# Performance work log

Hardware: AMD Instinct MI355X
Metric: run time of the kernel (lower is better)

Reference implementation:

```python
import jax, jax.numpy as jnp
from jax import lax
import numpy as np

D, DI, S, K, R = 128, 256, 16, 4, 8  # d_model, d_inner, d_state, d_conv, dt_rank
B, W, N, E = 8, 64, 128, 256


def _ln(x, g, b, eps=1e-5):
    m = x.mean(-1, keepdims=True)
    v = ((x - m) ** 2).mean(-1, keepdims=True)
    return (x - m) * lax.rsqrt(v + eps) * g + b


def _mamba(x, w_in, conv_w, conv_b, w_xp, dt_w, dt_b, Alog, Dp, w_out):
    # x: (Bq, W, D) -> (Bq, W, D). Faithful mamba_ssm.Mamba math (selective scan).
    Bq, Wlen, _ = x.shape
    xz = x @ w_in                       # (Bq, W, 2*DI)
    xc, z = jnp.split(xz, 2, axis=-1)
    # causal depthwise conv over time
    xt = xc.transpose(0, 2, 1)          # (Bq, DI, W)
    xt = lax.conv_general_dilated(xt, conv_w[:, None, :], (1,), [(K - 1, 0)],
                                  feature_group_count=DI)
    xc = jax.nn.silu(xt + conv_b[None, :, None]).transpose(0, 2, 1)  # (Bq, W, DI)
    dbc = xc @ w_xp                     # (Bq, W, R+2S)
    dt = jax.nn.softplus(dbc[..., :R] @ dt_w + dt_b)   # (Bq, W, DI)
    Bm = dbc[..., R:R + S]              # (Bq, W, S)
    Cm = dbc[..., R + S:]               # (Bq, W, S)
    A = -jnp.exp(Alog)                  # (DI, S)

    def step(h, inp):
        dt_t, B_t, C_t, x_t = inp       # (Bq,DI),(Bq,S),(Bq,S),(Bq,DI)
        dA = jnp.exp(dt_t[..., None] * A)                 # (Bq,DI,S)
        h = dA * h + (dt_t * x_t)[..., None] * B_t[:, None, :]
        y = jnp.einsum('bds,bs->bd', h, C_t)
        return h, y

    h0 = jnp.zeros((Bq, DI, S), x.dtype)
    _, ys = lax.scan(step, h0, (dt.transpose(1, 0, 2), Bm.transpose(1, 0, 2),
                                Cm.transpose(1, 0, 2), xc.transpose(1, 0, 2)))
    y = ys.transpose(1, 0, 2) + xc * Dp          # D skip connection
    y = y * jax.nn.silu(z)
    return y @ w_out


def _forward(x_node, x_trace, x_log, mp_in, mp_conv_w, mp_conv_b, mp_xproj,
             mp_dt_w, mp_dt_b, mp_Alog, mp_D, mp_out, mix_w, mix_b,
             an_g, an_b, ff1_w, ff1_b, ff2_w, ff2_b, fln_g, fln_b):
    Bz, Wz, Nz, _ = x_node.shape
    Ez = x_trace.shape[2]
    # (B,W,N,D) -> (B*N, W, D) per-entity temporal sequences
    sn = x_node.transpose(0, 2, 1, 3).reshape(Bz * Nz, Wz, D)
    st = x_trace.transpose(0, 2, 1, 3).reshape(Bz * Ez, Wz, D)
    sl = x_log.transpose(0, 2, 1, 3).reshape(Bz * Nz, Wz, D)

    def mam(i, s):
        return _mamba(s, mp_in[i], mp_conv_w[i], mp_conv_b[i], mp_xproj[i],
                      mp_dt_w[i], mp_dt_b[i], mp_Alog[i], mp_D[i], mp_out[i])

    yn, yt, yl = mam(0, sn), mam(1, st), mam(2, sl)

    # cross-modal mixing of node & log with residual (dropout = identity in eval)
    cat = jnp.concatenate([yn, yl], axis=-1)          # (B*N, W, 2D)
    cat = cat + jax.nn.silu(cat @ mix_w + mix_b)
    yn, yl = jnp.split(cat, 2, axis=-1)

    # back to (B, W, N/E, D)
    yn = yn.reshape(Bz, Nz, Wz, D).transpose(0, 2, 1, 3)
    yt = yt.reshape(Bz, Ez, Wz, D).transpose(0, 2, 1, 3)
    yl = yl.reshape(Bz, Nz, Wz, D).transpose(0, 2, 1, 3)

    # AddALL: AddNorm(old, new) = LN(dropout(new) + old)
    n1 = _ln(yn + x_node, an_g[0], an_b[0])
    t1 = _ln(yt + x_trace, an_g[1], an_b[1])
    l1 = _ln(yl + x_log, an_g[2], an_b[2])

    # FFN: AddNorm(x, FeedForward(x)) per modality, LeakyReLU(0.01)
    def ffn(i, x):
        h = jax.nn.leaky_relu(x @ ff1_w[i] + ff1_b[i], 0.01)
        return _ln(h @ ff2_w[i] + ff2_b[i] + x, fln_g[i], fln_b[i])

    n2, t2, l2 = ffn(0, n1), ffn(1, t1), ffn(2, l1)
    # concat along entity axis (all feature dims = D) for a single output
    return jnp.concatenate([n2, t2, l2], axis=2)      # (B, W, 2N+E, D)


def setup_inputs() -> dict:
    key = jax.random.key(0)
    ks = jax.random.split(key, 16)
    f = lambda k, shp, s=1.0: jax.random.normal(k, shp, dtype=jnp.float32) * s
    return {
        'x_node': f(ks[0], (B, W, N, D)),
        'x_trace': f(ks[1], (B, W, E, D)),
        'x_log': f(ks[2], (B, W, N, D)),
        'mp_in': f(ks[3], (3, D, 2 * DI), 0.05),
        'mp_conv_w': f(ks[4], (3, DI, K), 0.2),
        'mp_conv_b': jnp.zeros((3, DI), jnp.float32),
        'mp_xproj': f(ks[5], (3, DI, R + 2 * S), 0.05),
        'mp_dt_w': f(ks[6], (3, R, DI), 0.1),
        'mp_dt_b': jnp.full((3, DI), float(np.log(np.expm1(0.01))), jnp.float32),
        'mp_Alog': jnp.log(jnp.broadcast_to(jnp.arange(1, S + 1, dtype=jnp.float32), (3, DI, S))),
        'mp_D': jnp.ones((3, DI), jnp.float32),
        'mp_out': f(ks[7], (3, DI, D), 0.05),
        'mix_w': f(ks[8], (2 * D, 2 * D), 0.05),
        'mix_b': jnp.zeros((2 * D,), jnp.float32),
        'an_g': jnp.ones((3, D), jnp.float32),
        'an_b': jnp.zeros((3, D), jnp.float32),
        'ff1_w': f(ks[9], (3, D, 4 * D), 0.05),
        'ff1_b': jnp.zeros((3, 4 * D), jnp.float32),
        'ff2_w': f(ks[10], (3, 4 * D, D), 0.05),
        'ff2_b': jnp.zeros((3, D), jnp.float32),
        'fln_g': jnp.ones((3, D), jnp.float32),
        'fln_b': jnp.zeros((3, D), jnp.float32),
    }


def reference(x_node, x_trace, x_log, mp_in, mp_conv_w, mp_conv_b, mp_xproj,
              mp_dt_w, mp_dt_b, mp_Alog, mp_D, mp_out, mix_w, mix_b,
              an_g, an_b, ff1_w, ff1_b, ff2_w, ff2_b, fln_g, fln_b):
    return _forward(x_node, x_trace, x_log, mp_in, mp_conv_w, mp_conv_b,
                    mp_xproj, mp_dt_w, mp_dt_b, mp_Alog, mp_D, mp_out,
                    mix_w, mix_b, an_g, an_b, ff1_w, ff1_b, ff2_w, ff2_b,
                    fln_g, fln_b)
```

## Files before the change

kernel.cpp:

```cpp
#include <hip/hip_runtime.h>
#include <hip/hip_bf16.h>

#define DEV __device__ __forceinline__

typedef __attribute__((ext_vector_type(8))) short bf16x8;
typedef __attribute__((ext_vector_type(4))) float f32x4;
typedef __attribute__((ext_vector_type(2))) float f32x2;

DEV f32x4 MF(bf16x8 a, bf16x8 b, f32x4 c) {
  return __builtin_amdgcn_mfma_f32_16x16x32_bf16(a, b, c, 0, 0, 0);
}

DEV float bf2f(unsigned short u) {
  union { unsigned int i; float f; } v; v.i = ((unsigned int)u) << 16; return v.f;
}
DEV unsigned short f2bf(float f) {
  __hip_bfloat16 h = __float2bfloat16(f);
  unsigned short r; __builtin_memcpy(&r, &h, 2); return r;
}
DEV unsigned int packbf(float a, float b) {
  float2 p; p.x = a; p.y = b;
  __hip_bfloat162 h = __float22bfloat162_rn(p);
  unsigned int r; __builtin_memcpy(&r, &h, 4); return r;
}
#define LOG2E 1.442695041f
#define LN2   0.6931471806f
DEV float silu_fast(float v) {
  float e = __builtin_amdgcn_exp2f(v * -LOG2E);
  return v * __builtin_amdgcn_rcpf(1.f + e);
}
DEV float softplus_fast(float v) {
  float e = __builtin_amdgcn_exp2f(v * LOG2E);
  float l = __builtin_amdgcn_logf(1.f + e) * LN2;
  return v > 15.f ? v : l;
}

#define WS_WINT   0
#define WS_WXPT   196608
#define WS_WOUTT  233472
#define WS_FF1T   331776
#define WS_FF2T   528384
#define WS_MIXT   724992
#define WS_TOTAL  790528

__global__ __launch_bounds__(256) void prep_kernel(
    const float* __restrict__ w_in, const float* __restrict__ w_xp,
    const float* __restrict__ w_out, const float* __restrict__ ff1,
    const float* __restrict__ ff2, const float* __restrict__ mixw,
    unsigned short* __restrict__ ws)
{
  int idx = blockIdx.x * 256 + threadIdx.x;
  if (idx >= WS_TOTAL) return;
  float v;
  if (idx < WS_WXPT) {
    int j = idx, s = j / 65536, r = j % 65536, n = r >> 7, k = r & 127;
    v = w_in[s * 65536 + k * 512 + n];
  } else if (idx < WS_WOUTT) {
    int j = idx - WS_WXPT, s = j / 12288, r = j % 12288, n = r >> 8, k = r & 255;
    v = (n < 40) ? w_xp[s * 10240 + k * 40 + n] : 0.f;
  } else if (idx < WS_FF1T) {
    int j = idx - WS_WOUTT, s = j / 32768, r = j % 32768, n = r >> 8, k = r & 255;
    v = w_out[s * 32768 + k * 128 + n];
  } else if (idx < WS_FF2T) {
    int j = idx - WS_FF1T, s = j / 65536, r = j % 65536, n = r >> 7, k = r & 127;
    v = ff1[s * 65536 + k * 512 + n];
  } else if (idx < WS_MIXT) {
    int j = idx - WS_FF2T, s = j / 65536, r = j % 65536, n = r >> 9, k = r & 511;
    v = ff2[s * 65536 + k * 128 + n];
  } else {
    int j = idx - WS_MIXT, n = j >> 8, k = j & 255;
    v = mixw[k * 256 + n];
  }
  ws[idx] = f2bf(v);
}

__global__ __launch_bounds__(256, 2) void mamba_front(
    const float* __restrict__ xn, const float* __restrict__ xt,
    const float* __restrict__ xl,
    const unsigned short* __restrict__ w_inT_all,
    const float* __restrict__ conv_w_all, const float* __restrict__ conv_b_all,
    const unsigned short* __restrict__ w_xpT_all,
    const float* __restrict__ dt_w_all, const float* __restrict__ dt_b_all,
    const float* __restrict__ Alog_all, const float* __restrict__ Dp_all,
    const unsigned short* __restrict__ w_outT_all,
    const float* __restrict__ an_g, const float* __restrict__ an_b,
    float* __restrict__ out)
{
  __shared__ __attribute__((aligned(16))) unsigned short xcz[64 * 512];
  __shared__ __attribute__((aligned(16))) char aux[16384];
  unsigned short* xs = (unsigned short*)aux;
  float* dbc = (float*)aux;

  const int tid = threadIdx.x;
  const int lane = tid & 63;
  const int wv = tid >> 6;
  const int lr = lane & 15;
  const int kg = lane >> 4;

  int blk = blockIdx.x, s, q;
  if (blk < 1024)      { s = 0; q = blk; }
  else if (blk < 3072) { s = 1; q = blk - 1024; }
  else                 { s = 2; q = blk - 3072; }
  const int SEQ = (s == 1) ? 256 : 128;
  const int slot_base = (s == 0) ? 0 : (s == 1 ? 128 : 384);
  const float* x = (s == 0) ? xn : (s == 1 ? xt : xl);
  const unsigned short* w_inT  = w_inT_all  + (size_t)s * 65536;
  const unsigned short* w_xpT  = w_xpT_all  + (size_t)s * 12288;
  const unsigned short* w_outT = w_outT_all + (size_t)s * 32768;
  const float* conv_w = conv_w_all + s * 1024;
  const float* conv_b = conv_b_all + s * 256;
  const float* dt_w   = dt_w_all + s * 2048;
  const float* dt_b   = dt_b_all + s * 256;
  const float* Alog   = Alog_all + s * 4096;
  const float* Dp     = Dp_all + s * 256;

  const int b = q / SEQ, n = q - b * SEQ;
  const float* xb = x + ((size_t)b * 64 * SEQ + n) * 128;

  for (int idx = tid; idx < 2048; idx += 256) {
    int t = idx >> 5, qd = (idx & 31) << 2;
    float4 v = *(const float4*)(xb + (size_t)t * SEQ * 128 + qd);
    uint2 p;
    p.x = packbf(v.x, v.y);
    p.y = packbf(v.z, v.w);
    *(uint2*)(&xs[t * 128 + (qd ^ ((t & 7) << 3))]) = p;
  }
  __syncthreads();

  {
    bf16x8 bx[4][4];
#pragma unroll
    for (int jt = 0; jt < 4; ++jt)
#pragma unroll
      for (int ks = 0; ks < 4; ++ks) {
        int t = jt * 16 + lr;
        bx[jt][ks] = *(const bf16x8*)(&xs[t * 128 + ((ks * 32 + kg * 8) ^ ((t & 7) << 3))]);
      }
    const int nb = wv * 128;
#pragma unroll
    for (int at = 0; at < 8; ++at) {
      bf16x8 av[4];
      int arow = nb + at * 16 + lr;
#pragma unroll
      for (int ks = 0; ks < 4; ++ks)
        av[ks] = *(const bf16x8*)(w_inT + arow * 128 + ks * 32 + kg * 8);
#pragma unroll
      for (int jt = 0; jt < 4; ++jt) {
        f32x4 c = {0.f, 0.f, 0.f, 0.f};
#pragma unroll
        for (int ks = 0; ks < 4; ++ks) c = MF(av[ks], bx[jt][ks], c);
        int t = jt * 16 + lr;
        int n0 = nb + at * 16 + kg * 4;
        uint2 p;
        p.x = packbf(c[0], c[1]);
        p.y = packbf(c[2], c[3]);
        *(uint2*)(&xcz[t * 512 + (n0 ^ ((t & 7) << 3))]) = p;
      }
    }
  }
  __syncthreads();

  {
    const int d = tid;
    float cw0 = conv_w[d * 4 + 0], cw1 = conv_w[d * 4 + 1];
    float cw2 = conv_w[d * 4 + 2], cw3 = conv_w[d * 4 + 3];
    float cb = conv_b[d];
    float xm3 = 0.f, xm2 = 0.f, xm1 = 0.f;
    for (int c0 = 0; c0 < 64; c0 += 16) {
      float xv[16];
#pragma unroll
      for (int u = 0; u < 16; ++u) {
        int t = c0 + u;
        xv[u] = bf2f(xcz[t * 512 + (d ^ ((t & 7) << 3))]);
      }
#pragma unroll
      for (int u = 0; u < 16; ++u) {
        float sv = fmaf(cw0, xm3, fmaf(cw1, xm2, fmaf(cw2, xm1, fmaf(cw3, xv[u], cb))));
        xm3 = xm2; xm2 = xm1; xm1 = xv[u];
        xv[u] = silu_fast(sv);
      }
#pragma unroll
      for (int u = 0; u < 16; ++u) {
        int t = c0 + u;
        xcz[t * 512 + (d ^ ((t & 7) << 3))] = f2bf(xv[u]);
      }
    }
  }
  __syncthreads();

  {
    bf16x8 av[8];
    int ta = wv * 16 + lr;
#pragma unroll
    for (int ks = 0; ks < 8; ++ks)
      av[ks] = *(const bf16x8*)(&xcz[ta * 512 + ((ks * 32 + kg * 8) ^ ((ta & 7) << 3))]);
#pragma unroll
    for (int ct = 0; ct < 3; ++ct) {
      f32x4 c = {0.f, 0.f, 0.f, 0.f};
#pragma unroll
      for (int ks = 0; ks < 8; ++ks) {
        bf16x8 bv = *(const bf16x8*)(w_xpT + (ct * 16 + lr) * 256 + ks * 32 + kg * 8);
        c = MF(av[ks], bv, c);
      }
      int tt = wv * 16 + kg * 4;
#pragma unroll
      for (int r = 0; r < 4; ++r)
        dbc[(tt + r) * 48 + ct * 16 + lr] = c[r];
    }
  }
  __syncthreads();

  {
    const int d = tid;
    float dtw[8];
#pragma unroll
    for (int r = 0; r < 8; ++r) dtw[r] = dt_w[r * 256 + d];
    const float dtb = dt_b[d];
    float Af2[16];
#pragma unroll
    for (int s2 = 0; s2 < 16; ++s2)
      Af2[s2] = -__builtin_amdgcn_exp2f(Alog[d * 16 + s2] * LOG2E) * LOG2E;
    const float af0l2 = Af2[0];
    bool geo = true;
#pragma unroll
    for (int s2 = 1; s2 < 16; ++s2)
      geo = geo && (fabsf(Af2[s2] - (float)(s2 + 1) * af0l2) <= 2e-4f * fabsf(Af2[s2]));
    const float Dv = Dp[d];

    const int eoff = d;
    const int zoff = 256 + d;

    if (geo) {
      f32x2 h2[8];
#pragma unroll
      for (int k = 0; k < 8; ++k) h2[k] = (f32x2){0.f, 0.f};
#pragma unroll 2
      for (int t = 0; t < 64; ++t) {
        const f32x4* dr4 = (const f32x4*)&dbc[t * 48];
        f32x4 d0 = dr4[0], d1 = dr4[1];
        float dtv = dtb;
        dtv = fmaf(dtw[0], d0[0], dtv); dtv = fmaf(dtw[1], d0[1], dtv);
        dtv = fmaf(dtw[2], d0[2], dtv); dtv = fmaf(dtw[3], d0[3], dtv);
        dtv = fmaf(dtw[4], d1[0], dtv); dtv = fmaf(dtw[5], d1[1], dtv);
        dtv = fmaf(dtw[6], d1[2], dtv); dtv = fmaf(dtw[7], d1[3], dtv);
        dtv = softplus_fast(dtv);
        int sw = (t & 7) << 3;
        int e = t * 512 + (eoff ^ sw);
        float xv = bf2f(xcz[e]);
        float zf = bf2f(xcz[t * 512 + (zoff ^ sw)]);
        float cf = dtv * xv;
        float r1 = __builtin_amdgcn_exp2f(dtv * af0l2);
        float r2 = r1 * r1;
        f32x2 r2v = {r2, r2};
        f32x2 pp = {r1, r2};
        f32x2 cf2 = {cf, cf};
        f32x2 y2 = {0.f, 0.f};
        f32x4 B0 = dr4[2], B1 = dr4[3], B2 = dr4[4], B3 = dr4[5];
        f32x4 C0 = dr4[6], C1 = dr4[7], C2 = dr4[8], C3 = dr4[9];
        f32x2 Bv[8] = {{B0[0],B0[1]},{B0[2],B0[3]},{B1[0],B1[1]},{B1[2],B1[3]},
                       {B2[0],B2[1]},{B2[2],B2[3]},{B3[0],B3[1]},{B3[2],B3[3]}};
        f32x2 Cv[8] = {{C0[0],C0[1]},{C0[2],C0[3]},{C1[0],C1[1]},{C1[2],C1[3]},
                       {C2[0],C2[1]},{C2[2],C2[3]},{C3[0],C3[1]},{C3[2],C3[3]}};
#pragma unroll
        for (int k = 0; k < 8; ++k) {
          h2[k] = __builtin_elementwise_fma(pp, h2[k], cf2 * Bv[k]);
          y2 = __builtin_elementwise_fma(h2[k], Cv[k], y2);
          pp = pp * r2v;
        }
        float y = y2[0] + y2[1];
        xcz[e] = f2bf((fmaf(xv, Dv, y)) * silu_fast(zf));
      }
    } else {
      float h[16];
#pragma unroll
      for (int s2 = 0; s2 < 16; ++s2) h[s2] = 0.f;
#pragma unroll 2
      for (int t = 0; t < 64; ++t) {
        const float* dr = &dbc[t * 48];
        float dtv = dtb;
#pragma unroll
        for (int r = 0; r < 8; ++r) dtv = fmaf(dtw[r], dr[r], dtv);
        dtv = softplus_fast(dtv);
        int sw = (t & 7) << 3;
        int e = t * 512 + (eoff ^ sw);
        float xv = bf2f(xcz[e]);
        float zf = bf2f(xcz[t * 512 + (zoff ^ sw)]);
        float cf = dtv * xv;
        float y = 0.f;
#pragma unroll
        for (int s2 = 0; s2 < 16; ++s2) {
          float dA = __builtin_amdgcn_exp2f(dtv * Af2[s2]);
          h[s2] = fmaf(dA, h[s2], cf * dr[8 + s2]);
          y = fmaf(h[s2], dr[24 + s2], y);
        }
        xcz[e] = f2bf((fmaf(xv, Dv, y)) * silu_fast(zf));
      }
    }
  }
  __syncthreads();

  {
    bf16x8 av[8];
    int ta = wv * 16 + lr;
#pragma unroll
    for (int ks = 0; ks < 8; ++ks)
      av[ks] = *(const bf16x8*)(&xcz[ta * 512 + ((ks * 32 + kg * 8) ^ ((ta & 7) << 3))]);
    f32x4 acc[8];
#pragma unroll
    for (int ct = 0; ct < 8; ++ct) {
      f32x4 c = {0.f, 0.f, 0.f, 0.f};
#pragma unroll
      for (int ks = 0; ks < 8; ++ks) {
        bf16x8 bv = *(const bf16x8*)(w_outT + (ct * 16 + lr) * 256 + ks * 32 + kg * 8);
        c = MF(av[ks], bv, c);
      }
      acc[ct] = c;
    }
    size_t ob = (size_t)b * 64 * 512 * 128 + (size_t)(slot_base + n) * 128;
    const int trow = wv * 16 + kg * 4;
    if (s != 1) {
#pragma unroll
      for (int ct = 0; ct < 8; ++ct) {
        int cc = ct * 16 + lr;
#pragma unroll
        for (int r = 0; r < 4; ++r)
          out[ob + (size_t)(trow + r) * 65536 + cc] = acc[ct][r];
      }
    } else {
      float sum[4] = {0.f, 0.f, 0.f, 0.f}, sq[4] = {0.f, 0.f, 0.f, 0.f};
#pragma unroll
      for (int ct = 0; ct < 8; ++ct) {
        int col = ct * 16 + lr;
#pragma unroll
        for (int r = 0; r < 4; ++r) {
          int t = trow + r;
          float xr = xb[(size_t)t * SEQ * 128 + col];
          float v = acc[ct][r] + xr;
          acc[ct][r] = v;
          sum[r] += v; sq[r] += v * v;
        }
      }
      float mn[4], rstd[4];
#pragma unroll
      for (int r = 0; r < 4; ++r) {
        float s1 = sum[r], s2 = sq[r];
        s1 += __shfl_xor(s1, 1); s2 += __shfl_xor(s2, 1);
        s1 += __shfl_xor(s1, 2); s2 += __shfl_xor(s2, 2);
        s1 += __shfl_xor(s1, 4); s2 += __shfl_xor(s2, 4);
        s1 += __shfl_xor(s1, 8); s2 += __shfl_xor(s2, 8);
        float mean = s1 * (1.f / 128.f);
        float var = s2 * (1.f / 128.f) - mean * mean;
        mn[r] = mean;
        rstd[r] = rsqrtf(var + 1e-5f);
      }
      const float* G  = an_g + 128;
      const float* Bv = an_b + 128;
#pragma unroll
      for (int ct = 0; ct < 8; ++ct) {
        int col = ct * 16 + lr;
        float gc = G[col], bc = Bv[col];
#pragma unroll
        for (int r = 0; r < 4; ++r)
          out[ob + (size_t)(trow + r) * 65536 + col] = (acc[ct][r] - mn[r]) * rstd[r] * gc + bc;
      }
    }
  }
}

__global__ __launch_bounds__(256, 4) void mix_kernel(
    float* __restrict__ out, const unsigned short* __restrict__ mixT,
    const float* __restrict__ mix_b,
    const float* __restrict__ xn, const float* __restrict__ xl,
    const float* __restrict__ an_g, const float* __restrict__ an_b)
{
  __shared__ __attribute__((aligned(16))) unsigned short cs[64 * 256];

  const int tid = threadIdx.x;
  const int lane = tid & 63;
  const int wv = tid >> 6;
  const int lr = lane & 15;
  const int kg = lane >> 4;
  const int bn = blockIdx.x;
  const int b = bn >> 7, n = bn & 127;
  const size_t base_n = (((size_t)b * 64) * 512 + n) * 128;
  const size_t base_l = (((size_t)b * 64) * 512 + 384 + n) * 128;

  for (int idx = tid; idx < 4096; idx += 256) {
    int t = idx >> 6, r = idx & 63;
    int half = r >> 5, qd = (r & 31) << 2;
    const float* src = out + (half ? base_l : base_n) + (size_t)t * 65536 + qd;
    float4 v = *(const float4*)src;
    int col = half * 128 + qd;
    uint2 p;
    p.x = packbf(v.x, v.y);
    p.y = packbf(v.z, v.w);
    *(uint2*)(&cs[t * 256 + (col ^ ((t & 7) << 3))]) = p;
  }
  __syncthreads();

  bf16x8 av[8];
  int ta = wv * 16 + lr;
#pragma unroll
  for (int ks = 0; ks < 8; ++ks)
    av[ks] = *(const bf16x8*)(&cs[ta * 256 + ((ks * 32 + kg * 8) ^ ((ta & 7) << 3))]);

  const int trow = wv * 16 + kg * 4;
#pragma unroll
  for (int half = 0; half < 2; ++half) {
    const float* xres_base = half ? xl : xn;
    f32x4 acc[8];
#pragma unroll
    for (int ct = 0; ct < 8; ++ct) {
      f32x4 c = {0.f, 0.f, 0.f, 0.f};
      int colg = half * 128 + ct * 16 + lr;
#pragma unroll
      for (int ks = 0; ks < 8; ++ks) {
        bf16x8 bv = *(const bf16x8*)(mixT + colg * 256 + ks * 32 + kg * 8);
        c = MF(av[ks], bv, c);
      }
      acc[ct] = c;
    }
    float sum[4] = {0.f, 0.f, 0.f, 0.f}, sq[4] = {0.f, 0.f, 0.f, 0.f};
#pragma unroll
    for (int ct = 0; ct < 8; ++ct) {
      int col = ct * 16 + lr;
      int colg = half * 128 + col;
      float bcol = mix_b[colg];
#pragma unroll
      for (int r = 0; r < 4; ++r) {
        int t = trow + r;
        float orig = bf2f(cs[t * 256 + (colg ^ ((t & 7) << 3))]);
        float xr = xres_base[(((size_t)b * 64 + t) * 128 + n) * 128 + col];
        float v = orig + silu_fast(acc[ct][r] + bcol) + xr;
        acc[ct][r] = v;
        sum[r] += v; sq[r] += v * v;
      }
    }
    float mn[4], rstd[4];
#pragma unroll
    for (int r = 0; r < 4; ++r) {
      float s1 = sum[r], s2 = sq[r];
      s1 += __shfl_xor(s1, 1); s2 += __shfl_xor(s2, 1);
      s1 += __shfl_xor(s1, 2); s2 += __shfl_xor(s2, 2);
      s1 += __shfl_xor(s1, 4); s2 += __shfl_xor(s2, 4);
      s1 += __shfl_xor(s1, 8); s2 += __shfl_xor(s2, 8);
      float mean = s1 * (1.f / 128.f);
      float var = s2 * (1.f / 128.f) - mean * mean;
      mn[r] = mean;
      rstd[r] = rsqrtf(var + 1e-5f);
    }
    const float* G  = an_g + (half ? 256 : 0);
    const float* Bv = an_b + (half ? 256 : 0);
    size_t base = half ? base_l : base_n;
#pragma unroll
    for (int ct = 0; ct < 8; ++ct) {
      int col = ct * 16 + lr;
      float gc = G[col], bc = Bv[col];
#pragma unroll
      for (int r = 0; r < 4; ++r)
        out[base + (size_t)(trow + r) * 65536 + col] = (acc[ct][r] - mn[r]) * rstd[r] * gc + bc;
    }
  }
}

__global__ __launch_bounds__(256, 2) void ffn_kernel(
    float* __restrict__ out,
    const unsigned short* __restrict__ ff1T, const float* __restrict__ b1,
    const unsigned short* __restrict__ ff2T, const float* __restrict__ b2,
    const float* __restrict__ g, const float* __restrict__ bb)
{
  __shared__ __attribute__((aligned(16))) unsigned short hT[64 * 512];
  __shared__ __attribute__((aligned(16))) unsigned short xs[64 * 128];

  const int tid = threadIdx.x;
  const int lane = tid & 63;
  const int wv = tid >> 6;
  const int lr = lane & 15;
  const int kg = lane >> 4;
  const int tok0 = blockIdx.x * 64;
  const int slot0 = tok0 & 511;
  const int s = slot0 < 128 ? 0 : (slot0 < 384 ? 1 : 2);
  const unsigned short* F1 = ff1T + (size_t)s * 65536;
  const unsigned short* F2 = ff2T + (size_t)s * 65536;
  const float* B1 = b1 + s * 512;
  const float* B2 = b2 + s * 128;
  const float* G = g + s * 128;
  const float* Bb = bb + s * 128;

  for (int idx = tid; idx < 2048; idx += 256) {
    int t = idx >> 5, qd = (idx & 31) << 2;
    float4 v = *(const float4*)(out + (size_t)(tok0 + t) * 128 + qd);
    uint2 p;
    p.x = packbf(v.x, v.y);
    p.y = packbf(v.z, v.w);
    *(uint2*)(&xs[t * 128 + (qd ^ ((t & 7) << 3))]) = p;
  }
  __syncthreads();

  {
    bf16x8 bx[4][4];
#pragma unroll
    for (int jt = 0; jt < 4; ++jt)
#pragma unroll
      for (int ks = 0; ks < 4; ++ks) {
        int t = jt * 16 + lr;
        bx[jt][ks] = *(const bf16x8*)(&xs[t * 128 + ((ks * 32 + kg * 8) ^ ((t & 7) << 3))]);
      }
    const int nb = wv * 128;
#pragma unroll
    for (int at = 0; at < 8; ++at) {
      bf16x8 av[4];
      int arow = nb + at * 16 + lr;
#pragma unroll
      for (int ks = 0; ks < 4; ++ks)
        av[ks] = *(const bf16x8*)(F1 + arow * 128 + ks * 32 + kg * 8);
      float4 bias = *(const float4*)(B1 + nb + at * 16 + kg * 4);
#pragma unroll
      for (int jt = 0; jt < 4; ++jt) {
        f32x4 c = {0.f, 0.f, 0.f, 0.f};
#pragma unroll
        for (int ks = 0; ks < 4; ++ks) c = MF(av[ks], bx[jt][ks], c);
        float v0 = c[0] + bias.x; v0 = v0 > 0.f ? v0 : 0.01f * v0;
        float v1 = c[1] + bias.y; v1 = v1 > 0.f ? v1 : 0.01f * v1;
        float v2 = c[2] + bias.z; v2 = v2 > 0.f ? v2 : 0.01f * v2;
        float v3 = c[3] + bias.w; v3 = v3 > 0.f ? v3 : 0.01f * v3;
        int t = jt * 16 + lr;
        int n0 = nb + at * 16 + kg * 4;
        uint2 p;
        p.x = packbf(v0, v1);
        p.y = packbf(v2, v3);
        *(uint2*)(&hT[t * 512 + (n0 ^ ((t & 7) << 3))]) = p;
      }
    }
  }
  __syncthreads();

  {
    bf16x8 av[16];
    int ta = wv * 16 + lr;
#pragma unroll
    for (int ks = 0; ks < 16; ++ks)
      av[ks] = *(const bf16x8*)(&hT[ta * 512 + ((ks * 32 + kg * 8) ^ ((ta & 7) << 3))]);
    f32x4 acc[8];
#pragma unroll
    for (int ct = 0; ct < 8; ++ct) {
      f32x4 c = {0.f, 0.f, 0.f, 0.f};
#pragma unroll
      for (int ks = 0; ks < 16; ++ks) {
        bf16x8 bv = *(const bf16x8*)(F2 + (ct * 16 + lr) * 512 + ks * 32 + kg * 8);
        c = MF(av[ks], bv, c);
      }
      acc[ct] = c;
    }

    float v[8][4];
    float sum[4] = {0.f, 0.f, 0.f, 0.f}, sq[4] = {0.f, 0.f, 0.f, 0.f};
    const int trow = wv * 16 + kg * 4;
#pragma unroll
    for (int ct = 0; ct < 8; ++ct) {
      int col = ct * 16 + lr;
      float b2c = B2[col];
#pragma unroll
      for (int r = 0; r < 4; ++r) {
        int t = trow + r;
        float xr = bf2f(xs[t * 128 + (col ^ ((t & 7) << 3))]);
        float val = acc[ct][r] + b2c + xr;
        v[ct][r] = val;
        sum[r] += val; sq[r] += val * val;
      }
    }
    float mn[4], rstd[4];
#pragma unroll
    for (int r = 0; r < 4; ++r) {
      float s1 = sum[r], s2 = sq[r];
      s1 += __shfl_xor(s1, 1); s2 += __shfl_xor(s2, 1);
      s1 += __shfl_xor(s1, 2); s2 += __shfl_xor(s2, 2);
      s1 += __shfl_xor(s1, 4); s2 += __shfl_xor(s2, 4);
      s1 += __shfl_xor(s1, 8); s2 += __shfl_xor(s2, 8);
      float mean = s1 * (1.f / 128.f);
      float var = s2 * (1.f / 128.f) - mean * mean;
      mn[r] = mean;
      rstd[r] = rsqrtf(var + 1e-5f);
    }
#pragma unroll
    for (int ct = 0; ct < 8; ++ct) {
      int col = ct * 16 + lr;
      float gc = G[col], bc = Bb[col];
#pragma unroll
      for (int r = 0; r < 4; ++r)
        out[(size_t)(tok0 + trow + r) * 128 + col] = (v[ct][r] - mn[r]) * rstd[r] * gc + bc;
    }
  }
}

extern "C" void kernel_launch(void* const* d_in, const int* in_sizes, int n_in,
                              void* d_out, int out_size, void* d_ws, size_t ws_size,
                              hipStream_t stream) {
  (void)in_sizes; (void)n_in; (void)out_size; (void)ws_size;
  const float* x_node  = (const float*)d_in[0];
  const float* x_trace = (const float*)d_in[1];
  const float* x_log   = (const float*)d_in[2];
  const float* mp_in     = (const float*)d_in[3];
  const float* mp_conv_w = (const float*)d_in[4];
  const float* mp_conv_b = (const float*)d_in[5];
  const float* mp_xproj  = (const float*)d_in[6];
  const float* mp_dt_w   = (const float*)d_in[7];
  const float* mp_dt_b   = (const float*)d_in[8];
  const float* mp_Alog   = (const float*)d_in[9];
  const float* mp_D      = (const float*)d_in[10];
  const float* mp_out    = (const float*)d_in[11];
  const float* mix_w = (const float*)d_in[12];
  const float* mix_b = (const float*)d_in[13];
  const float* an_g  = (const float*)d_in[14];
  const float* an_b  = (const float*)d_in[15];
  const float* ff1_w = (const float*)d_in[16];
  const float* ff1_b = (const float*)d_in[17];
  const float* ff2_w = (const float*)d_in[18];
  const float* ff2_b = (const float*)d_in[19];
  const float* fln_g = (const float*)d_in[20];
  const float* fln_b = (const float*)d_in[21];
  float* out = (float*)d_out;

  unsigned short* ws = (unsigned short*)d_ws;

  prep_kernel<<<(WS_TOTAL + 255) / 256, 256, 0, stream>>>(
      mp_in, mp_xproj, mp_out, ff1_w, ff2_w, mix_w, ws);

  mamba_front<<<4096, 256, 0, stream>>>(
      x_node, x_trace, x_log,
      ws + WS_WINT, mp_conv_w, mp_conv_b, ws + WS_WXPT,
      mp_dt_w, mp_dt_b, mp_Alog, mp_D, ws + WS_WOUTT,
      an_g, an_b, out);

  mix_kernel<<<1024, 256, 0, stream>>>(out, ws + WS_MIXT, mix_b,
                                       x_node, x_log, an_g, an_b);

  ffn_kernel<<<4096, 256, 0, stream>>>(out, ws + WS_FF1T, ff1_b,
                                       ws + WS_FF2T, ff2_b, fln_g, fln_b);
}
```

Before: 801.4 us.

## Fuse FFN into mamba trace path and mix kernel, dropping separate FFN launch

The FFN block (ff1, leaky-relu, ff2, residual, layernorm) is now computed in-kernel. For the trace stream it runs in mamba_front, reusing shared memory for the hidden activations; for node and log it runs inside a combined mix+FFN kernel, which splits the 512-wide hidden dimension into two halves to fit shared memory. This removes the FFN kernel launch and its global round-trip of the full activation tensor. In exchange, register and LDS pressure rises in both kernels, which can lower occupancy, and the mix kernel now serialises more work per block across only 1024 blocks.

```diff
diff --git a/kernel.cpp b/kernel.cpp
--- a/kernel.cpp
+++ b/kernel.cpp
@@ -84,6 +84,9 @@
     const float* __restrict__ Alog_all, const float* __restrict__ Dp_all,
     const unsigned short* __restrict__ w_outT_all,
     const float* __restrict__ an_g, const float* __restrict__ an_b,
+    const unsigned short* __restrict__ ff1T, const float* __restrict__ fb1,
+    const unsigned short* __restrict__ ff2T, const float* __restrict__ fb2,
+    const float* __restrict__ fln_g, const float* __restrict__ fln_b,
     float* __restrict__ out)
 {
   __shared__ __attribute__((aligned(16))) unsigned short xcz[64 * 512];
@@ -360,20 +363,127 @@
         int col = ct * 16 + lr;
         float gc = G[col], bc = Bv[col];
 #pragma unroll
-        for (int r = 0; r < 4; ++r)
-          out[ob + (size_t)(trow + r) * 65536 + col] = (acc[ct][r] - mn[r]) * rstd[r] * gc + bc;
-      }
-    }
-  }
-}
-
-__global__ __launch_bounds__(256, 4) void mix_kernel(
+        for (int r = 0; r < 4; ++r) {
+          int t = trow + r;
+          float t1 = (acc[ct][r] - mn[r]) * rstd[r] * gc + bc;
+          xs[t * 128 + (col ^ ((t & 7) << 3))] = f2bf(t1);
+        }
+      }
+      __syncthreads();
+
+      const unsigned short* F1 = ff1T + 65536;
+      const unsigned short* F2 = ff2T + 65536;
+      const float* B1 = fb1 + 512;
+      const float* B2 = fb2 + 128;
+      const float* FG = fln_g + 128;
+      const float* FB = fln_b + 128;
+      {
+        bf16x8 bx[4][4];
+#pragma unroll
+        for (int jt = 0; jt < 4; ++jt)
+#pragma unroll
+          for (int ks = 0; ks < 4; ++ks) {
+            int t = jt * 16 + lr;
+            bx[jt][ks] = *(const bf16x8*)(&xs[t * 128 + ((ks * 32 + kg * 8) ^ ((t & 7) << 3))]);
+          }
+        const int nb = wv * 128;
+#pragma unroll
+        for (int at = 0; at < 8; ++at) {
+          bf16x8 av1[4];
+          int arow = nb + at * 16 + lr;
+#pragma unroll
+          for (int ks = 0; ks < 4; ++ks)
+            av1[ks] = *(const bf16x8*)(F1 + arow * 128 + ks * 32 + kg * 8);
+          float4 bias = *(const float4*)(B1 + nb + at * 16 + kg * 4);
+#pragma unroll
+          for (int jt = 0; jt < 4; ++jt) {
+            f32x4 c = {0.f, 0.f, 0.f, 0.f};
+#pragma unroll
+            for (int ks = 0; ks < 4; ++ks) c = MF(av1[ks], bx[jt][ks], c);
+            float v0 = c[0] + bias.x; v0 = v0 > 0.f ? v0 : 0.01f * v0;
+            float v1 = c[1] + bias.y; v1 = v1 > 0.f ? v1 : 0.01f * v1;
+            float v2 = c[2] + bias.z; v2 = v2 > 0.f ? v2 : 0.01f * v2;
+            float v3 = c[3] + bias.w; v3 = v3 > 0.f ? v3 : 0.01f * v3;
+            int t = jt * 16 + lr;
+            int n0 = nb + at * 16 + kg * 4;
+            uint2 p;
+            p.x = packbf(v0, v1);
+            p.y = packbf(v2, v3);
+            *(uint2*)(&xcz[t * 512 + (n0 ^ ((t & 7) << 3))]) = p;
+          }
+        }
+      }
+      __syncthreads();
+      {
+        bf16x8 av2[16];
+        int ta2 = wv * 16 + lr;
+#pragma unroll
+        for (int ks = 0; ks < 16; ++ks)
+          av2[ks] = *(const bf16x8*)(&xcz[ta2 * 512 + ((ks * 32 + kg * 8) ^ ((ta2 & 7) << 3))]);
+        f32x4 a2[8];
+#pragma unroll
+        for (int ct = 0; ct < 8; ++ct) {
+          f32x4 c = {0.f, 0.f, 0.f, 0.f};
+#pragma unroll
+          for (int ks = 0; ks < 16; ++ks) {
+            bf16x8 bv = *(const bf16x8*)(F2 + (ct * 16 + lr) * 512 + ks * 32 + kg * 8);
+            c = MF(av2[ks], bv, c);
+          }
+          a2[ct] = c;
+        }
+        float vv[8][4];
+        float su[4] = {0.f, 0.f, 0.f, 0.f}, sb[4] = {0.f, 0.f, 0.f, 0.f};
+#pragma unroll
+        for (int ct = 0; ct < 8; ++ct) {
+          int col = ct * 16 + lr;
+          float b2c = B2[col];
+#pragma unroll
+          for (int r = 0; r < 4; ++r) {
+            int t = trow + r;
+            float xr = bf2f(xs[t * 128 + (col ^ ((t & 7) << 3))]);
+            float val = a2[ct][r] + b2c + xr;
+            vv[ct][r] = val;
+            su[r] += val; sb[r] += val * val;
+          }
+        }
+        float mn2[4], rs2[4];
+#pragma unroll
+        for (int r = 0; r < 4; ++r) {
+          float s1 = su[r], s2 = sb[r];
+          s1 += __shfl_xor(s1, 1); s2 += __shfl_xor(s2, 1);
+          s1 += __shfl_xor(s1, 2); s2 += __shfl_xor(s2, 2);
+          s1 += __shfl_xor(s1, 4); s2 += __shfl_xor(s2, 4);
+          s1 += __shfl_xor(s1, 8); s2 += __shfl_xor(s2, 8);
+          float mean = s1 * (1.f / 128.f);
+          float var = s2 * (1.f / 128.f) - mean * mean;
+          mn2[r] = mean;
+          rs2[r] = rsqrtf(var + 1e-5f);
+        }
+#pragma unroll
+        for (int ct = 0; ct < 8; ++ct) {
+          int col = ct * 16 + lr;
+          float gc = FG[col], bc = FB[col];
+#pragma unroll
+          for (int r = 0; r < 4; ++r)
+            out[ob + (size_t)(trow + r) * 65536 + col] = (vv[ct][r] - mn2[r]) * rs2[r] * gc + bc;
+        }
+      }
+    }
+  }
+}
+
+__global__ __launch_bounds__(256, 2) void mix_ffn_kernel(
     float* __restrict__ out, const unsigned short* __restrict__ mixT,
     const float* __restrict__ mix_b,
     const float* __restrict__ xn, const float* __restrict__ xl,
-    const float* __restrict__ an_g, const float* __restrict__ an_b)
+    const float* __restrict__ an_g, const float* __restrict__ an_b,
+    const unsigned short* __restrict__ ff1T, const float* __restrict__ fb1,
+    const unsigned short* __restrict__ ff2T, const float* __restrict__ fb2,
+    const float* __restrict__ fln_g, const float* __restrict__ fln_b)
 {
   __shared__ __attribute__((aligned(16))) unsigned short cs[64 * 256];
+  __shared__ __attribute__((aligned(16))) unsigned short xs[64 * 128];
+  __shared__ __attribute__((aligned(16))) unsigned short hT[64 * 256];
 
   const int tid = threadIdx.x;
   const int lane = tid & 63;
@@ -407,6 +517,7 @@
   const int trow = wv * 16 + kg * 4;
 #pragma unroll
   for (int half = 0; half < 2; ++half) {
+    const int sf = half ? 2 : 0;
     const float* xres_base = half ? xl : xn;
     f32x4 acc[8];
 #pragma unroll
@@ -449,55 +560,30 @@
       mn[r] = mean;
       rstd[r] = rsqrtf(var + 1e-5f);
     }
-    const float* G  = an_g + (half ? 256 : 0);
-    const float* Bv = an_b + (half ? 256 : 0);
-    size_t base = half ? base_l : base_n;
-#pragma unroll
-    for (int ct = 0; ct < 8; ++ct) {
-      int col = ct * 16 + lr;
-      float gc = G[col], bc = Bv[col];
-#pragma unroll
-      for (int r = 0; r < 4; ++r)
-        out[base + (size_t)(trow + r) * 65536 + col] = (acc[ct][r] - mn[r]) * rstd[r] * gc + bc;
-    }
-  }
-}
-
-__global__ __launch_bounds__(256, 2) void ffn_kernel(
-    float* __restrict__ out,
-    const unsigned short* __restrict__ ff1T, const float* __restrict__ b1,
-    const unsigned short* __restrict__ ff2T, const float* __restrict__ b2,
-    const float* __restrict__ g, const float* __restrict__ bb)
-{
-  __shared__ __attribute__((aligned(16))) unsigned short hT[64 * 512];
-  __shared__ __attribute__((aligned(16))) unsigned short xs[64 * 128];
-
-  const int tid = threadIdx.x;
-  const int lane = tid & 63;
-  const int wv = tid >> 6;
-  const int lr = lane & 15;
-  const int kg = lane >> 4;
-  const int tok0 = blockIdx.x * 64;
-  const int slot0 = tok0 & 511;
-  const int s = slot0 < 128 ? 0 : (slot0 < 384 ? 1 : 2);
-  const unsigned short* F1 = ff1T + (size_t)s * 65536;
-  const unsigned short* F2 = ff2T + (size_t)s * 65536;
-  const float* B1 = b1 + s * 512;
-  const float* B2 = b2 + s * 128;
-  const float* G = g + s * 128;
-  const float* Bb = bb + s * 128;
-
-  for (int idx = tid; idx < 2048; idx += 256) {
-    int t = idx >> 5, qd = (idx & 31) << 2;
-    float4 v = *(const float4*)(out + (size_t)(tok0 + t) * 128 + qd);
-    uint2 p;
-    p.x = packbf(v.x, v.y);
-    p.y = packbf(v.z, v.w);
-    *(uint2*)(&xs[t * 128 + (qd ^ ((t & 7) << 3))]) = p;
-  }
-  __syncthreads();
-
-  {
+    {
+      const float* G  = an_g + (half ? 256 : 0);
+      const float* Bv = an_b + (half ? 256 : 0);
+#pragma unroll
+      for (int ct = 0; ct < 8; ++ct) {
+        int col = ct * 16 + lr;
+        float gc = G[col], bc = Bv[col];
+#pragma unroll
+        for (int r = 0; r < 4; ++r) {
+          int t = trow + r;
+          float n1 = (acc[ct][r] - mn[r]) * rstd[r] * gc + bc;
+          xs[t * 128 + (col ^ ((t & 7) << 3))] = f2bf(n1);
+        }
+      }
+    }
+    __syncthreads();
+
+    const unsigned short* F1 = ff1T + (size_t)sf * 65536;
+    const unsigned short* F2 = ff2T + (size_t)sf * 65536;
+    const float* B1 = fb1 + sf * 512;
+    const float* B2 = fb2 + sf * 128;
+    const float* FG = fln_g + sf * 128;
+    const float* FB = fln_b + sf * 128;
+
     bf16x8 bx[4][4];
 #pragma unroll
     for (int jt = 0; jt < 4; ++jt)
@@ -506,90 +592,98 @@
         int t = jt * 16 + lr;
         bx[jt][ks] = *(const bf16x8*)(&xs[t * 128 + ((ks * 32 + kg * 8) ^ ((t & 7) << 3))]);
       }
-    const int nb = wv * 128;
-#pragma unroll
-    for (int at = 0; at < 8; ++at) {
-      bf16x8 av[4];
-      int arow = nb + at * 16 + lr;
-#pragma unroll
-      for (int ks = 0; ks < 4; ++ks)
-        av[ks] = *(const bf16x8*)(F1 + arow * 128 + ks * 32 + kg * 8);
-      float4 bias = *(const float4*)(B1 + nb + at * 16 + kg * 4);
-#pragma unroll
-      for (int jt = 0; jt < 4; ++jt) {
-        f32x4 c = {0.f, 0.f, 0.f, 0.f};
-#pragma unroll
-        for (int ks = 0; ks < 4; ++ks) c = MF(av[ks], bx[jt][ks], c);
-        float v0 = c[0] + bias.x; v0 = v0 > 0.f ? v0 : 0.01f * v0;
-        float v1 = c[1] + bias.y; v1 = v1 > 0.f ? v1 : 0.01f * v1;
-        float v2 = c[2] + bias.z; v2 = v2 > 0.f ? v2 : 0.01f * v2;
-        float v3 = c[3] + bias.w; v3 = v3 > 0.f ? v3 : 0.01f * v3;
-        int t = jt * 16 + lr;
-        int n0 = nb + at * 16 + kg * 4;
-        uint2 p;
-        p.x = packbf(v0, v1);
-        p.y = packbf(v2, v3);
-        *(uint2*)(&hT[t * 512 + (n0 ^ ((t & 7) << 3))]) = p;
-      }
-    }
-  }
-  __syncthreads();
-
-  {
-    bf16x8 av[16];
-    int ta = wv * 16 + lr;
-#pragma unroll
-    for (int ks = 0; ks < 16; ++ks)
-      av[ks] = *(const bf16x8*)(&hT[ta * 512 + ((ks * 32 + kg * 8) ^ ((ta & 7) << 3))]);
-    f32x4 acc[8];
-#pragma unroll
-    for (int ct = 0; ct < 8; ++ct) {
-      f32x4 c = {0.f, 0.f, 0.f, 0.f};
-#pragma unroll
-      for (int ks = 0; ks < 16; ++ks) {
-        bf16x8 bv = *(const bf16x8*)(F2 + (ct * 16 + lr) * 512 + ks * 32 + kg * 8);
-        c = MF(av[ks], bv, c);
-      }
-      acc[ct] = c;
-    }
-
-    float v[8][4];
-    float sum[4] = {0.f, 0.f, 0.f, 0.f}, sq[4] = {0.f, 0.f, 0.f, 0.f};
-    const int trow = wv * 16 + kg * 4;
-#pragma unroll
-    for (int ct = 0; ct < 8; ++ct) {
-      int col = ct * 16 + lr;
-      float b2c = B2[col];
+
+    f32x4 acc2[8];
+#pragma unroll
+    for (int ct = 0; ct < 8; ++ct) acc2[ct] = (f32x4){0.f, 0.f, 0.f, 0.f};
+
+#pragma unroll
+    for (int kh = 0; kh < 2; ++kh) {
+      const int nb = kh * 256 + wv * 64;
+#pragma unroll
+      for (int at = 0; at < 4; ++at) {
+        bf16x8 av1[4];
+        int arow = nb + at * 16 + lr;
+#pragma unroll
+        for (int ks = 0; ks < 4; ++ks)
+          av1[ks] = *(const bf16x8*)(F1 + arow * 128 + ks * 32 + kg * 8);
+        float4 bias = *(const float4*)(B1 + nb + at * 16 + kg * 4);
+#pragma unroll
+        for (int jt = 0; jt < 4; ++jt) {
+          f32x4 c = {0.f, 0.f, 0.f, 0.f};
+#pragma unroll
+          for (int ks = 0; ks < 4; ++ks) c = MF(av1[ks], bx[jt][ks], c);
+          float v0 = c[0] + bias.x; v0 = v0 > 0.f ? v0 : 0.01f * v0;
+          float v1 = c[1] + bias.y; v1 = v1 > 0.f ? v1 : 0.01f * v1;
+          float v2 = c[2] + bias.z; v2 = v2 > 0.f ? v2 : 0.01f * v2;
+          float v3 = c[3] + bias.w; v3 = v3 > 0.f ? v3 : 0.01f * v3;
+          int t = jt * 16 + lr;
+          int nl = wv * 64 + at * 16 + kg * 4;
+          uint2 p;
+          p.x = packbf(v0, v1);
+          p.y = packbf(v2, v3);
+          *(uint2*)(&hT[t * 256 + (nl ^ ((t & 7) << 3))]) = p;
+        }
+      }
+      __syncthreads();
+
+      bf16x8 av2[8];
+#pragma unroll
+      for (int ks = 0; ks < 8; ++ks)
+        av2[ks] = *(const bf16x8*)(&hT[ta * 256 + ((ks * 32 + kg * 8) ^ ((ta & 7) << 3))]);
+#pragma unroll
+      for (int ct = 0; ct < 8; ++ct) {
+        f32x4 c = acc2[ct];
+#pragma unroll
+        for (int ks = 0; ks < 8; ++ks) {
+          bf16x8 bv = *(const bf16x8*)(F2 + (ct * 16 + lr) * 512 + kh * 256 + ks * 32 + kg * 8);
+          c = MF(av2[ks], bv, c);
+        }
+        acc2[ct] = c;
+      }
+      __syncthreads();
+    }
+
+    {
+      float vv[8][4];
+      float su[4] = {0.f, 0.f, 0.f, 0.f}, sb[4] = {0.f, 0.f, 0.f, 0.f};
+#pragma unroll
+      for (int ct = 0; ct < 8; ++ct) {
+        int col = ct * 16 + lr;
+        float b2c = B2[col];
+#pragma unroll
+        for (int r = 0; r < 4; ++r) {
+          int t = trow + r;
+          float xr = bf2f(xs[t * 128 + (col ^ ((t & 7) << 3))]);
+          float val = acc2[ct][r] + b2c + xr;
+          vv[ct][r] = val;
+          su[r] += val; sb[r] += val * val;
+        }
+      }
+      float mn2[4], rs2[4];
 #pragma unroll
       for (int r = 0; r < 4; ++r) {
-        int t = trow + r;
-        float xr = bf2f(xs[t * 128 + (col ^ ((t & 7) << 3))]);
-        float val = acc[ct][r] + b2c + xr;
-        v[ct][r] = val;
-        sum[r] += val; sq[r] += val * val;
-      }
-    }
-    float mn[4], rstd[4];
-#pragma unroll
-    for (int r = 0; r < 4; ++r) {
-      float s1 = sum[r], s2 = sq[r];
-      s1 += __shfl_xor(s1, 1); s2 += __shfl_xor(s2, 1);
-      s1 += __shfl_xor(s1, 2); s2 += __shfl_xor(s2, 2);
-      s1 += __shfl_xor(s1, 4); s2 += __shfl_xor(s2, 4);
-      s1 += __shfl_xor(s1, 8); s2 += __shfl_xor(s2, 8);
-      float mean = s1 * (1.f / 128.f);
-      float var = s2 * (1.f / 128.f) - mean * mean;
-      mn[r] = mean;
-      rstd[r] = rsqrtf(var + 1e-5f);
-    }
-#pragma unroll
-    for (int ct = 0; ct < 8; ++ct) {
-      int col = ct * 16 + lr;
-      float gc = G[col], bc = Bb[col];
-#pragma unroll
-      for (int r = 0; r < 4; ++r)
-        out[(size_t)(tok0 + trow + r) * 128 + col] = (v[ct][r] - mn[r]) * rstd[r] * gc + bc;
-    }
+        float s1 = su[r], s2 = sb[r];
+        s1 += __shfl_xor(s1, 1); s2 += __shfl_xor(s2, 1);
+        s1 += __shfl_xor(s1, 2); s2 += __shfl_xor(s2, 2);
+        s1 += __shfl_xor(s1, 4); s2 += __shfl_xor(s2, 4);
+        s1 += __shfl_xor(s1, 8); s2 += __shfl_xor(s2, 8);
+        float mean = s1 * (1.f / 128.f);
+        float var = s2 * (1.f / 128.f) - mean * mean;
+        mn2[r] = mean;
+        rs2[r] = rsqrtf(var + 1e-5f);
+      }
+      size_t base = half ? base_l : base_n;
+#pragma unroll
+      for (int ct = 0; ct < 8; ++ct) {
+        int col = ct * 16 + lr;
+        float gc = FG[col], bc = FB[col];
+#pragma unroll
+        for (int r = 0; r < 4; ++r)
+          out[base + (size_t)(trow + r) * 65536 + col] = (vv[ct][r] - mn2[r]) * rs2[r] * gc + bc;
+      }
+    }
+    __syncthreads();
   }
 }
 
@@ -630,11 +724,11 @@
       x_node, x_trace, x_log,
       ws + WS_WINT, mp_conv_w, mp_conv_b, ws + WS_WXPT,
       mp_dt_w, mp_dt_b, mp_Alog, mp_D, ws + WS_WOUTT,
-      an_g, an_b, out);
-
-  mix_kernel<<<1024, 256, 0, stream>>>(out, ws + WS_MIXT, mix_b,
-                                       x_node, x_log, an_g, an_b);
-
-  ffn_kernel<<<4096, 256, 0, stream>>>(out, ws + WS_FF1T, ff1_b,
-                                       ws + WS_FF2T, ff2_b, fln_g, fln_b);
-}
+      an_g, an_b,
+      ws + WS_FF1T, ff1_b, ws + WS_FF2T, ff2_b, fln_g, fln_b,
+      out);
+
+  mix_ffn_kernel<<<1024, 256, 0, stream>>>(
+      out, ws + WS_MIXT, mix_b, x_node, x_log, an_g, an_b,
+      ws + WS_FF1T, ff1_b, ws + WS_FF2T, ff2_b, fln_g, fln_b);
+}
```

After: 792.9 us (median of 2 runs). Within noise of the previous version (-1.1%).
